# Kernel tuning notes

Measured on AMD Instinct MI355X. Metric: run time of the kernel, lower is better.

The kernel has to match this reference:

```python
import jax, jax.numpy as jnp
import numpy as np

EPS_PAR = 1e-12
EPS_PT = 1e-12
LOSS_EPS = 1e-3


def edge_edge_distance(p1, q1, p2, q2, eps=EPS_PAR):
    # p1,q1,p2,q2: (N,3); returns (N,) min distance between segments
    d1 = q1 - p1
    d2 = q2 - p2
    r = p1 - p2
    a = (d1 * d1).sum(1)
    e = (d2 * d2).sum(1)
    f = (d2 * r).sum(1)
    b = (d1 * d2).sum(1)
    c = (d1 * r).sum(1)
    denom = a * e - b * b
    parallel = denom < eps
    denom_adj = jnp.where(parallel, jnp.ones_like(denom), denom)
    s = (b * f - c * e) / denom_adj
    t = (a * f - b * c) / denom_adj
    s = jnp.where(parallel, jnp.zeros_like(s), s)
    s_cl = jnp.clip(s, 0.0, 1.0)
    t_cl = jnp.clip(t, 0.0, 1.0)
    recompute_t = (s_cl != s) | parallel
    r_new = r + s_cl[:, None] * d1
    t_new = jnp.clip((r_new * d2).sum(1) / e, 0.0, 1.0)
    t_fin = jnp.where(recompute_t, t_new, t_cl)
    recompute_s = (t_cl != t) & (~parallel) & (s_cl == s)
    r_new2 = r - t_fin[:, None] * d2
    s_new = (-r_new2 * d1).sum(1) / a
    s_fin = jnp.where(recompute_s, jnp.clip(s_new, 0.0, 1.0), s_cl)
    c1 = p1 + s_fin[:, None] * d1
    c2 = p2 + t_fin[:, None] * d2
    diff = c1 - c2
    return jnp.sqrt((diff * diff).sum(1))


def point_triangle_distance(point, tri):
    # Faithful to original: slices tri along the LAST (coordinate) axis.
    v0, v1, v2 = tri[:, :, 0], tri[:, :, 1], tri[:, :, 2]
    e0 = v1 - v0
    e1 = v2 - v0
    w = point - v0
    a = jnp.maximum((e0 * e0).sum(1), EPS_PT)
    b = (e0 * e1).sum(1)
    c = jnp.maximum((e1 * e1).sum(1), EPS_PT)
    d = (e0 * w).sum(1)
    e = (e1 * w).sum(1)
    f = (w * w).sum(1)
    det = jnp.maximum(a * c - b * b, EPS_PT)
    s = b * e - c * d
    t = b * d - a * e
    in_face = (s >= 0) & (t >= 0) & (s + t <= det)
    s01 = jnp.clip(d / a, 0.0, 1.0)
    d2_e01 = ((w - s01[:, None] * e0) ** 2).sum(1)
    t02 = jnp.clip(e / c, 0.0, 1.0)
    d2_e02 = ((w - t02[:, None] * e1) ** 2).sum(1)
    w2 = point - v1
    e2 = v2 - v1
    a2 = jnp.maximum((e2 * e2).sum(1), EPS_PT)
    dd2 = (e2 * w2).sum(1)
    u12 = jnp.clip(dd2 / a2, 0.0, 1.0)
    d2_e12 = ((w2 - u12[:, None] * e2) ** 2).sum(1)
    d2_face = jnp.maximum((f * det - (d * s + e * t)) / det, 0.0)
    dist2 = jnp.where(in_face, d2_face, jnp.minimum(jnp.minimum(d2_e01, d2_e02), d2_e12))
    return jnp.sqrt(dist2)


def triangle_distance(tp, otp):
    # tp, otp: (N,3,3)
    min_dist = jnp.full((tp.shape[0],), jnp.inf, dtype=tp.dtype)
    for i in range(3):
        min_dist = jnp.minimum(min_dist, point_triangle_distance(tp[:, i], otp))
        min_dist = jnp.minimum(min_dist, point_triangle_distance(otp[:, i], tp))
    for i in range(3):
        for j in range(3):
            min_dist = jnp.minimum(
                min_dist,
                edge_edge_distance(tp[:, i], tp[:, (i + 1) % 3], otp[:, j], otp[:, (j + 1) % 3]),
            )
    return min_dist


def setup_inputs() -> dict:
    key = jax.random.key(0)
    k1, k2 = jax.random.split(key)
    B, F, P = 4, 50000, 500000
    triangles = jax.random.normal(k1, (B, F, 3, 3), dtype=jnp.float32)
    close_idxs = jax.random.randint(k2, (B, P, 2), 0, F, dtype=jnp.int64)
    return {"triangles": triangles, "close_idxs": close_idxs}


def reference(triangles, close_idxs):
    B, P = close_idxs.shape[0], close_idxs.shape[1]
    recv_f = close_idxs[..., 0].reshape(-1)
    intr_f = close_idxs[..., 1].reshape(-1)
    batch = jnp.repeat(jnp.arange(B), P)
    valid = (recv_f >= 0).astype(triangles.dtype)
    recv_f = jnp.maximum(recv_f, 0)
    intr_f = jnp.maximum(intr_f, 0)
    recv_tri = triangles[batch, recv_f]  # (N,3,3)
    intr_tri = triangles[batch, intr_f]  # (N,3,3)
    dist = triangle_distance(recv_tri, intr_tri)
    pen = jnp.maximum(LOSS_EPS - dist, 0.0)
    # masked mean == torch .mean() over the selected (valid) close pairs
    loss = jnp.sum(pen * valid) / jnp.maximum(jnp.sum(valid), 1.0)
    return loss
```

## Files before the change

### kernel.cpp

```cpp
#include <hip/hip_runtime.h>

#define LOSS_EPS 0.001f
#define EPS_PAR 1e-12f
#define EPS_PT 1e-12f

typedef float f32x2 __attribute__((ext_vector_type(2)));
typedef int   i32x2 __attribute__((ext_vector_type(2)));

__device__ __forceinline__ f32x2 vmin2(f32x2 a, f32x2 b) { return __builtin_elementwise_min(a, b); }
__device__ __forceinline__ f32x2 vmax2(f32x2 a, f32x2 b) { return __builtin_elementwise_max(a, b); }
__device__ __forceinline__ f32x2 vclamp01(f32x2 v) {
    return vmin2(vmax2(v, (f32x2)0.0f), (f32x2)1.0f);
}
__device__ __forceinline__ f32x2 vrcp(f32x2 x) {
    f32x2 r; r.x = __builtin_amdgcn_rcpf(x.x); r.y = __builtin_amdgcn_rcpf(x.y); return r;
}
__device__ __forceinline__ f32x2 vsel(i32x2 m, f32x2 a, f32x2 b) {
    i32x2 ai = __builtin_bit_cast(i32x2, a);
    i32x2 bi = __builtin_bit_cast(i32x2, b);
    i32x2 r = (ai & m) | (bi & ~m);
    return __builtin_bit_cast(f32x2, r);
}

struct V3p { f32x2 x, y, z; };
__device__ __forceinline__ V3p operator-(V3p a, V3p b) { return {a.x - b.x, a.y - b.y, a.z - b.z}; }
__device__ __forceinline__ V3p operator+(V3p a, V3p b) { return {a.x + b.x, a.y + b.y, a.z + b.z}; }
__device__ __forceinline__ V3p operator*(f32x2 s, V3p a) { return {s * a.x, s * a.y, s * a.z}; }
__device__ __forceinline__ f32x2 dotp(V3p a, V3p b) { return a.x * b.x + a.y * b.y + a.z * b.z; }

__device__ __forceinline__ f32x2 edge_edge_d2(V3p p1, V3p d1, V3p p2, V3p d2,
                                              f32x2 a, f32x2 e, f32x2 ra, f32x2 re) {
    V3p r = p1 - p2;
    f32x2 f = dotp(d2, r);
    f32x2 b = dotp(d1, d2);
    f32x2 c = dotp(d1, r);
    f32x2 denom = a * e - b * b;
    i32x2 par = denom < (f32x2)EPS_PAR;
    f32x2 rd = vrcp(vsel(par, (f32x2)1.0f, denom));
    f32x2 s = (b * f - c * e) * rd;
    f32x2 t = (a * f - b * c) * rd;
    s = vsel(par, (f32x2)0.0f, s);
    f32x2 s_cl = vclamp01(s);
    f32x2 t_cl = vclamp01(t);
    i32x2 rec_t = (s_cl != s) | par;
    V3p r_new = r + s_cl * d1;
    f32x2 t_new = vclamp01(dotp(r_new, d2) * re);
    f32x2 t_fin = vsel(rec_t, t_new, t_cl);
    i32x2 rec_s = (t_cl != t) & ~par & (s_cl == s);
    V3p r_new2 = r - t_fin * d2;
    f32x2 s_new = (-dotp(r_new2, d1)) * ra;
    f32x2 s_fin = vsel(rec_s, vclamp01(s_new), s_cl);
    V3p c1 = p1 + s_fin * d1;
    V3p c2 = p2 + t_fin * d2;
    V3p diff = c1 - c2;
    return dotp(diff, diff);
}

__device__ __forceinline__ f32x2 ptri3_min_d2(V3p p0, V3p p1, V3p p2,
                                              V3p v0, V3p v1, V3p v2) {
    V3p e0 = v1 - v0;
    V3p e1 = v2 - v0;
    V3p e2t = v2 - v1;
    f32x2 a  = vmax2(dotp(e0, e0), (f32x2)EPS_PT);
    f32x2 b  = dotp(e0, e1);
    f32x2 c  = vmax2(dotp(e1, e1), (f32x2)EPS_PT);
    f32x2 a2 = vmax2(dotp(e2t, e2t), (f32x2)EPS_PT);
    f32x2 det = vmax2(a * c - b * b, (f32x2)EPS_PT);
    f32x2 ra = vrcp(a), rc = vrcp(c), ra2 = vrcp(a2), rdet = vrcp(det);

    f32x2 best = (f32x2)1e30f;
    V3p pts[3] = {p0, p1, p2};
#pragma unroll
    for (int k = 0; k < 3; ++k) {
        V3p p = pts[k];
        V3p w = p - v0;
        f32x2 d = dotp(e0, w);
        f32x2 e = dotp(e1, w);
        f32x2 f = dotp(w, w);
        f32x2 s = b * e - c * d;
        f32x2 t = b * d - a * e;
        i32x2 in_face = (s >= (f32x2)0.0f) & (t >= (f32x2)0.0f) & ((s + t) <= det);
        f32x2 s01 = vclamp01(d * ra);
        V3p u01 = w - s01 * e0;
        f32x2 d2_e01 = dotp(u01, u01);
        f32x2 t02 = vclamp01(e * rc);
        V3p u02 = w - t02 * e1;
        f32x2 d2_e02 = dotp(u02, u02);
        V3p w2 = p - v1;
        f32x2 dd2 = dotp(e2t, w2);
        f32x2 u12 = vclamp01(dd2 * ra2);
        V3p u12v = w2 - u12 * e2t;
        f32x2 d2_e12 = dotp(u12v, u12v);
        f32x2 d2_face = vmax2((f * det - (d * s + e * t)) * rdet, (f32x2)0.0f);
        f32x2 d2_edge = vmin2(vmin2(d2_e01, d2_e02), d2_e12);
        best = vmin2(best, vsel(in_face, d2_face, d2_edge));
    }
    return best;
}

__device__ __forceinline__ f32x2 body_from_T(const f32x2 T1[9], const f32x2 T2[9], f32x2 vmask) {
    V3p A[3]  = { {T1[0], T1[1], T1[2]}, {T1[3], T1[4], T1[5]}, {T1[6], T1[7], T1[8]} };
    V3p Ac[3] = { {T1[0], T1[3], T1[6]}, {T1[1], T1[4], T1[7]}, {T1[2], T1[5], T1[8]} };
    V3p B[3]  = { {T2[0], T2[1], T2[2]}, {T2[3], T2[4], T2[5]}, {T2[6], T2[7], T2[8]} };
    V3p Bc[3] = { {T2[0], T2[3], T2[6]}, {T2[1], T2[4], T2[7]}, {T2[2], T2[5], T2[8]} };

    f32x2 mind2 = (f32x2)1e30f;
    mind2 = vmin2(mind2, ptri3_min_d2(A[0], A[1], A[2], Bc[0], Bc[1], Bc[2]));
    mind2 = vmin2(mind2, ptri3_min_d2(B[0], B[1], B[2], Ac[0], Ac[1], Ac[2]));

    V3p dA[3] = { A[1] - A[0], A[2] - A[1], A[0] - A[2] };
    V3p dB[3] = { B[1] - B[0], B[2] - B[1], B[0] - B[2] };
    f32x2 la[3], lb[3], rla[3], rlb[3];
#pragma unroll
    for (int k = 0; k < 3; ++k) {
        la[k] = dotp(dA[k], dA[k]); rla[k] = vrcp(la[k]);
        lb[k] = dotp(dB[k], dB[k]); rlb[k] = vrcp(lb[k]);
    }
#pragma unroll
    for (int ii = 0; ii < 3; ++ii) {
#pragma unroll
        for (int jj = 0; jj < 3; ++jj) {
            mind2 = vmin2(mind2, edge_edge_d2(A[ii], dA[ii], B[jj], dB[jj],
                                              la[ii], lb[jj], rla[ii], rlb[jj]));
        }
    }
    f32x2 dist;
    dist.x = __builtin_sqrtf(mind2.x);
    dist.y = __builtin_sqrtf(mind2.y);
    return vmax2((f32x2)LOSS_EPS - dist, (f32x2)0.0f) * vmask;
}

__device__ __forceinline__ void block_reduce_atomic_fused(float pen, float val, float* ws,
                                                          float* out, unsigned nwg) {
#pragma unroll
    for (int off = 32; off > 0; off >>= 1) {
        pen += __shfl_down(pen, off);
        val += __shfl_down(val, off);
    }
    __shared__ float sp[4], sv[4];
    int wid = threadIdx.x >> 6;
    if ((threadIdx.x & 63) == 0) { sp[wid] = pen; sv[wid] = val; }
    __syncthreads();
    if (threadIdx.x == 0) {
        atomicAdd(&ws[0], sp[0] + sp[1] + sp[2] + sp[3]);
        atomicAdd(&ws[1], sv[0] + sv[1] + sv[2] + sv[3]);
        __threadfence();
        unsigned done = atomicAdd((unsigned*)(ws + 2), 1u);
        if (done == nwg - 1) {
            float p = atomicAdd(&ws[0], 0.0f);
            float v = atomicAdd(&ws[1], 0.0f);
            out[0] = p / fmaxf(v, 1.0f);
        }
    }
}

#define PPT 8
#define PAIRS_PER_BLOCK (256 * PPT)

__global__ void __launch_bounds__(256)
pen_loss_pipe2(const float* __restrict__ tris, const int* __restrict__ idx,
               float* __restrict__ ws, float* __restrict__ out,
               int npairs, int F, int P, int nwg) {
    int pb = blockIdx.x;
    int x = pb & 7, j = pb >> 3;
    int q8 = nwg >> 3, r8 = nwg & 7;
    int start = (x < r8) ? x * (q8 + 1) : r8 * (q8 + 1) + (x - r8) * q8;
    int lb = start + j;
    int tid = (int)threadIdx.x;
    int p0 = lb * PAIRS_PER_BLOCK + tid;

    int o1[PPT], o2[PPT];
    float vm[PPT];
#pragma unroll
    for (int k = 0; k < PPT; ++k) {
        int p = p0 + k * 256;
        int pc = min(p, npairs - 1);
        long long pr = __builtin_nontemporal_load((const long long*)idx + pc);
        int rx = (int)(pr & 0xffffffffLL);
        int ry = (int)(pr >> 32);
        vm[k] = (p < npairs && rx >= 0) ? 1.0f : 0.0f;
        int b = (pc >= P) + (pc >= 2 * P) + (pc >= 3 * P);
        int base = b * F;
        o1[k] = (base + max(rx, 0)) * 9;
        o2[k] = (base + max(ry, 0)) * 9;
    }

    float4 qAe0, qAe1, qBe0, qBe1, qAo0, qAo1, qBo0, qBo1;
    float  sAe, sBe, sAo, sBo;

#define LOADBODY(m) do {                                                      \
        const int ev = 2 * (m), od = 2 * (m) + 1;                             \
        qAe0 = *(const float4*)(tris + o1[ev]);                               \
        qAe1 = *(const float4*)(tris + o1[ev] + 4);                           \
        sAe  = tris[o1[ev] + 8];                                              \
        qBe0 = *(const float4*)(tris + o2[ev]);                               \
        qBe1 = *(const float4*)(tris + o2[ev] + 4);                           \
        sBe  = tris[o2[ev] + 8];                                              \
        qAo0 = *(const float4*)(tris + o1[od]);                               \
        qAo1 = *(const float4*)(tris + o1[od] + 4);                           \
        sAo  = tris[o1[od] + 8];                                              \
        qBo0 = *(const float4*)(tris + o2[od]);                               \
        qBo1 = *(const float4*)(tris + o2[od] + 4);                           \
        sBo  = tris[o2[od] + 8];                                              \
    } while (0)

#define PACKT(T1, T2) do {                                                    \
        T1[0] = (f32x2){qAe0.x, qAo0.x}; T1[1] = (f32x2){qAe0.y, qAo0.y};     \
        T1[2] = (f32x2){qAe0.z, qAo0.z}; T1[3] = (f32x2){qAe0.w, qAo0.w};     \
        T1[4] = (f32x2){qAe1.x, qAo1.x}; T1[5] = (f32x2){qAe1.y, qAo1.y};     \
        T1[6] = (f32x2){qAe1.z, qAo1.z}; T1[7] = (f32x2){qAe1.w, qAo1.w};     \
        T1[8] = (f32x2){sAe, sAo};                                            \
        T2[0] = (f32x2){qBe0.x, qBo0.x}; T2[1] = (f32x2){qBe0.y, qBo0.y};     \
        T2[2] = (f32x2){qBe0.z, qBo0.z}; T2[3] = (f32x2){qBe0.w, qBo0.w};     \
        T2[4] = (f32x2){qBe1.x, qBo1.x}; T2[5] = (f32x2){qBe1.y, qBo1.y};     \
        T2[6] = (f32x2){qBe1.z, qBo1.z}; T2[7] = (f32x2){qBe1.w, qBo1.w};     \
        T2[8] = (f32x2){sBe, sBo};                                            \
    } while (0)

    LOADBODY(0);
    f32x2 pen2 = (f32x2)0.0f;
#pragma unroll
    for (int m = 0; m < PPT / 2; ++m) {
        f32x2 T1[9], T2[9];
        PACKT(T1, T2);
        if (m < PPT / 2 - 1) LOADBODY(m + 1);
        f32x2 vmm = {vm[2 * m], vm[2 * m + 1]};
        pen2 += body_from_T(T1, T2, vmm);
    }
#undef LOADBODY
#undef PACKT

    float pen_s = pen2.x + pen2.y;
    float val_s = 0.0f;
#pragma unroll
    for (int k = 0; k < PPT; ++k) val_s += vm[k];
    block_reduce_atomic_fused(pen_s, val_s, ws, out, (unsigned)nwg);
}

extern "C" void kernel_launch(void* const* d_in, const int* in_sizes, int n_in,
                              void* d_out, int out_size, void* d_ws, size_t ws_size,
                              hipStream_t stream) {
    const float* tris = (const float*)d_in[0];
    const int* idx = (const int*)d_in[1];
    float* out = (float*)d_out;
    float* ws = (float*)d_ws;

    const int B = 4;
    int F = in_sizes[0] / (B * 9);
    int npairs = in_sizes[1] / 2;
    int P = npairs / B;

    hipMemsetAsync(d_ws, 0, 12, stream);
    int nwg = (npairs + PAIRS_PER_BLOCK - 1) / PAIRS_PER_BLOCK;
    pen_loss_pipe2<<<nwg, 256, 0, stream>>>(tris, idx, ws, out,
                                            npairs, F, P, nwg);
}
```

Baseline: 75.60 us.

## Repack triangles to aligned float4 layout inside a cooperative persistent kernel

Adds a cooperative kernel that first repacks each 9-float triangle into three 16-byte-aligned float4 slots in workspace. After a grid-wide sync, persistent blocks gather from the packed buffer with vector loads and evaluate the pair chunks. The final reduction uses a second grid sync instead of a completion counter. This trades an extra pass over the triangle array and two grid barriers for fewer, aligned gather loads. If workspace is too small or the cooperative launch fails, it falls back to the original direct kernel.

```diff
diff --git a/kernel.cpp b/kernel.cpp
--- a/kernel.cpp
+++ b/kernel.cpp
@@ -1,4 +1,7 @@
 #include <hip/hip_runtime.h>
+#include <hip/hip_cooperative_groups.h>
+
+namespace cg = cooperative_groups;
 
 #define LOSS_EPS 0.001f
 #define EPS_PAR 1e-12f
@@ -130,6 +133,126 @@
     return vmax2((f32x2)LOSS_EPS - dist, (f32x2)0.0f) * vmask;
 }
 
+#define PPT 8
+#define PAIRS_PER_BLOCK (256 * PPT)
+
+__device__ __forceinline__ void do_chunk(const float4* __restrict__ pack,
+                                         const int* __restrict__ idx,
+                                         int lb, int npairs, int F, int P,
+                                         float& pen_acc, float& val_acc) {
+    int tid = (int)threadIdx.x;
+    int p0 = lb * PAIRS_PER_BLOCK + tid;
+
+    int o1[PPT], o2[PPT];
+    float vm[PPT];
+#pragma unroll
+    for (int k = 0; k < PPT; ++k) {
+        int p = p0 + k * 256;
+        int pc = min(p, npairs - 1);
+        long long pr = __builtin_nontemporal_load((const long long*)idx + pc);
+        int rx = (int)(pr & 0xffffffffLL);
+        int ry = (int)(pr >> 32);
+        vm[k] = (p < npairs && rx >= 0) ? 1.0f : 0.0f;
+        int b = (pc >= P) + (pc >= 2 * P) + (pc >= 3 * P);
+        int base = b * F;
+        o1[k] = (base + max(rx, 0)) * 4;
+        o2[k] = (base + max(ry, 0)) * 4;
+    }
+
+    float4 qb_[12];
+#define LOADBODY(m) do {                                                      \
+        const int ev = 2 * (m), od = 2 * (m) + 1;                             \
+        qb_[0] = pack[o1[ev]];     qb_[1] = pack[o1[ev] + 1];                 \
+        qb_[2] = pack[o1[ev] + 2]; qb_[3] = pack[o2[ev]];                     \
+        qb_[4] = pack[o2[ev] + 1]; qb_[5] = pack[o2[ev] + 2];                 \
+        qb_[6] = pack[o1[od]];     qb_[7] = pack[o1[od] + 1];                 \
+        qb_[8] = pack[o1[od] + 2]; qb_[9] = pack[o2[od]];                     \
+        qb_[10] = pack[o2[od] + 1]; qb_[11] = pack[o2[od] + 2];               \
+    } while (0)
+
+#define PACKT(T1, T2) do {                                                    \
+        T1[0] = (f32x2){qb_[0].x, qb_[6].x}; T1[1] = (f32x2){qb_[0].y, qb_[6].y}; \
+        T1[2] = (f32x2){qb_[0].z, qb_[6].z}; T1[3] = (f32x2){qb_[0].w, qb_[6].w}; \
+        T1[4] = (f32x2){qb_[1].x, qb_[7].x}; T1[5] = (f32x2){qb_[1].y, qb_[7].y}; \
+        T1[6] = (f32x2){qb_[1].z, qb_[7].z}; T1[7] = (f32x2){qb_[1].w, qb_[7].w}; \
+        T1[8] = (f32x2){qb_[2].x, qb_[8].x};                                      \
+        T2[0] = (f32x2){qb_[3].x, qb_[9].x}; T2[1] = (f32x2){qb_[3].y, qb_[9].y}; \
+        T2[2] = (f32x2){qb_[3].z, qb_[9].z}; T2[3] = (f32x2){qb_[3].w, qb_[9].w}; \
+        T2[4] = (f32x2){qb_[4].x, qb_[10].x}; T2[5] = (f32x2){qb_[4].y, qb_[10].y}; \
+        T2[6] = (f32x2){qb_[4].z, qb_[10].z}; T2[7] = (f32x2){qb_[4].w, qb_[10].w}; \
+        T2[8] = (f32x2){qb_[5].x, qb_[11].x};                                     \
+    } while (0)
+
+    LOADBODY(0);
+    f32x2 pen2 = (f32x2)0.0f;
+#pragma unroll
+    for (int m = 0; m < PPT / 2; ++m) {
+        f32x2 T1[9], T2[9];
+        PACKT(T1, T2);
+        if (m < PPT / 2 - 1) LOADBODY(m + 1);
+        f32x2 vmm = {vm[2 * m], vm[2 * m + 1]};
+        pen2 += body_from_T(T1, T2, vmm);
+    }
+#undef LOADBODY
+#undef PACKT
+
+    pen_acc += pen2.x + pen2.y;
+#pragma unroll
+    for (int k = 0; k < PPT; ++k) val_acc += vm[k];
+}
+
+__global__ void __launch_bounds__(256)
+pen_loss_coop(const float* __restrict__ tris, const int* __restrict__ idx,
+              float4* __restrict__ pack, float* __restrict__ ws,
+              float* __restrict__ out, int npairs, int F, int P, int nchunks) {
+    cg::grid_group grid = cg::this_grid();
+    int tid = (int)threadIdx.x;
+    int gsz = (int)gridDim.x;
+    int ntri = 4 * F;
+
+    for (int g = (int)blockIdx.x * 256 + tid; g < ntri; g += gsz * 256) {
+        const float* s = tris + (size_t)g * 9;
+        float t[9];
+#pragma unroll
+        for (int k = 0; k < 9; ++k) t[k] = s[k];
+        float4* d = pack + (size_t)g * 4;
+        d[0] = make_float4(t[0], t[1], t[2], t[3]);
+        d[1] = make_float4(t[4], t[5], t[6], t[7]);
+        d[2] = make_float4(t[8], 0.0f, 0.0f, 0.0f);
+    }
+    grid.sync();
+
+    float pen_s = 0.0f, val_s = 0.0f;
+    int q8 = nchunks >> 3, r8 = nchunks & 7;
+    for (int pc = (int)blockIdx.x; pc < nchunks; pc += gsz) {
+        int x = pc & 7, j = pc >> 3;
+        int start = (x < r8) ? x * (q8 + 1) : r8 * (q8 + 1) + (x - r8) * q8;
+        int lb = start + j;
+        do_chunk(pack, idx, lb, npairs, F, P, pen_s, val_s);
+    }
+
+#pragma unroll
+    for (int off = 32; off > 0; off >>= 1) {
+        pen_s += __shfl_down(pen_s, off);
+        val_s += __shfl_down(val_s, off);
+    }
+    __shared__ float sp[4], sv[4];
+    int wid = tid >> 6;
+    if ((tid & 63) == 0) { sp[wid] = pen_s; sv[wid] = val_s; }
+    __syncthreads();
+    if (tid == 0) {
+        atomicAdd(&ws[0], sp[0] + sp[1] + sp[2] + sp[3]);
+        atomicAdd(&ws[1], sv[0] + sv[1] + sv[2] + sv[3]);
+    }
+    grid.sync();
+
+    if (blockIdx.x == 0 && tid == 0) {
+        float p = atomicAdd(&ws[0], 0.0f);
+        float v = atomicAdd(&ws[1], 0.0f);
+        out[0] = p / fmaxf(v, 1.0f);
+    }
+}
+
 __device__ __forceinline__ void block_reduce_atomic_fused(float pen, float val, float* ws,
                                                           float* out, unsigned nwg) {
 #pragma unroll
@@ -154,13 +277,10 @@
     }
 }
 
-#define PPT 8
-#define PAIRS_PER_BLOCK (256 * PPT)
-
 __global__ void __launch_bounds__(256)
-pen_loss_pipe2(const float* __restrict__ tris, const int* __restrict__ idx,
-               float* __restrict__ ws, float* __restrict__ out,
-               int npairs, int F, int P, int nwg) {
+pen_loss_direct(const float* __restrict__ tris, const int* __restrict__ idx,
+                float* __restrict__ ws, float* __restrict__ out,
+                int npairs, int F, int P, int nwg) {
     int pb = blockIdx.x;
     int x = pb & 7, j = pb >> 3;
     int q8 = nwg >> 3, r8 = nwg & 7;
@@ -249,9 +369,37 @@
     int F = in_sizes[0] / (B * 9);
     int npairs = in_sizes[1] / 2;
     int P = npairs / B;
-
-    hipMemsetAsync(d_ws, 0, 12, stream);
-    int nwg = (npairs + PAIRS_PER_BLOCK - 1) / PAIRS_PER_BLOCK;
-    pen_loss_pipe2<<<nwg, 256, 0, stream>>>(tris, idx, ws, out,
-                                            npairs, F, P, nwg);
-}
+    int ntri = B * F;
+    int nchunks = (npairs + PAIRS_PER_BLOCK - 1) / PAIRS_PER_BLOCK;
+
+    size_t need = 256 + (size_t)ntri * 64;
+    bool launched = false;
+
+    if (ws_size >= need) {
+        float4* pack = (float4*)((char*)d_ws + 256);
+        int blocksPerCU = 0;
+        hipError_t e1 = hipOccupancyMaxActiveBlocksPerMultiprocessor(
+            &blocksPerCU, (const void*)pen_loss_coop, 256, 0);
+        int numCU = 0;
+        hipError_t e2 = hipDeviceGetAttribute(&numCU,
+            hipDeviceAttributeMultiprocessorCount, 0);
+        if (e1 == hipSuccess && e2 == hipSuccess && blocksPerCU > 0 && numCU > 0) {
+            int maxBlocks = blocksPerCU * numCU;
+            int nb = nchunks < maxBlocks ? nchunks : maxBlocks;
+            hipMemsetAsync(d_ws, 0, 8, stream);
+            void* args[] = {(void*)&tris, (void*)&idx, (void*)&pack, (void*)&ws,
+                            (void*)&out, (void*)&npairs, (void*)&F, (void*)&P,
+                            (void*)&nchunks};
+            hipError_t e3 = hipLaunchCooperativeKernel((void*)pen_loss_coop,
+                                                       dim3(nb), dim3(256),
+                                                       args, 0, stream);
+            launched = (e3 == hipSuccess);
+        }
+    }
+
+    if (!launched) {
+        hipMemsetAsync(d_ws, 0, 12, stream);
+        pen_loss_direct<<<nchunks, 256, 0, stream>>>(tris, idx, ws, out,
+                                                     npairs, F, P, nchunks);
+    }
+}
```

Result: slower. 147.0 us (+94.4%).
